# Performance work log

Hardware: AMD Instinct MI355X
Metric: run time of the kernel (lower is better)

## Reference

```python
import jax, jax.numpy as jnp
import numpy as np

N = 100000      # nodes
E = 1600000     # edges (avg degree 16)
K = 3           # num_stacks
T = 4           # num_layers
H = 16          # hidden channels (conv1 out)
C = 1           # num_classes
BN_EPS = 1e-5


def setup_inputs() -> dict:
    key = jax.random.key(0)
    ks = jax.random.split(key, 14)
    s = 0.1
    return {
        "x": jax.random.normal(ks[0], (N, 1), jnp.float32),
        "edge_index": jax.random.randint(ks[1], (2, E), 0, N, dtype=jnp.int64),
        "edge_weight": jax.random.uniform(ks[2], (E,), jnp.float32),
        # conv1 (ARMAConv 1->16, K stacks, shared weights)
        "w1_init": jax.random.normal(ks[3], (K, 1, H), jnp.float32) * s,
        "w1_w":    jax.random.normal(ks[4], (K, H, H), jnp.float32) * s,
        "w1_root": jax.random.normal(ks[5], (K, 1, H), jnp.float32) * s,
        "w1_b":    jax.random.normal(ks[6], (K, H), jnp.float32) * s,
        "bn1_g": jnp.ones((H,), jnp.float32),
        "bn1_b": jnp.zeros((H,), jnp.float32),
        # conv2 (ARMAConv 16->1, act=None)
        "w2_init": jax.random.normal(ks[7], (K, H, C), jnp.float32) * s,
        "w2_w":    jax.random.normal(ks[8], (K, C, C), jnp.float32) * s,
        "w2_root": jax.random.normal(ks[9], (K, H, C), jnp.float32) * s,
        "w2_b":    jax.random.normal(ks[10], (K, C), jnp.float32) * s,
        # end linear 1->1
        "lin_w": jax.random.normal(ks[11], (C, C), jnp.float32) * s,
        "lin_b": jnp.zeros((C,), jnp.float32),
    }


def _arma_conv(x, src, dst, norm, init_w, w, root_w, bias, act):
    """PyG ARMAConv with shared weights. x: [N,Fin] -> [N,Fout]."""
    n = x.shape[0]
    # root/skip term (dropout is identity in eval); bias broadcast per stack
    root = jnp.einsum('ni,kio->nko', x, root_w) + bias[None, :, :]  # [N,K,Fout]
    out = jnp.einsum('ni,kio->nko', x, init_w)                      # t=0 transform
    for t in range(T):
        if t > 0:
            out = jnp.einsum('nki,kio->nko', out, w)                # shared weight
        msg = out[src] * norm[:, None, None]                        # [E,K,Fout]
        out = jax.ops.segment_sum(msg, dst, num_segments=n)         # A_hat @ out
        out = out + root
        if act:
            out = jax.nn.relu(out)
    return out.mean(axis=1)  # average over stacks


def reference(x, edge_index, edge_weight, w1_init, w1_w, w1_root, w1_b,
              bn1_g, bn1_b, w2_init, w2_w, w2_root, w2_b, lin_w, lin_b):
    src, dst = edge_index[0], edge_index[1]
    n = x.shape[0]
    # gcn_norm without self loops
    deg = jax.ops.segment_sum(edge_weight, dst, num_segments=n)
    dis = jnp.where(deg > 0, 1.0 / jnp.sqrt(deg), 0.0)
    norm = dis[src] * edge_weight * dis[dst]

    h = _arma_conv(x, src, dst, norm, w1_init, w1_w, w1_root, w1_b, act=True)
    # BatchNorm1d over node dim (batch statistics, deterministic)
    mu = h.mean(axis=0)
    var = h.var(axis=0)
    h = (h - mu) / jnp.sqrt(var + BN_EPS) * bn1_g + bn1_b
    h = jax.nn.relu(h)
    # dropout is identity in eval
    h = _arma_conv(h, src, dst, norm, w2_init, w2_w, w2_root, w2_b, act=False)
    h = h @ lin_w.T + lin_b
    return jax.nn.sigmoid(h)
```

## Files before the change

kernel.cpp:

```cpp
#include <hip/hip_runtime.h>
#include <hip/hip_bf16.h>
#include <hip/hip_fp16.h>
#include <math.h>

#define CAP 44

__device__ __forceinline__ float pk_w(unsigned pk) {
    return __half2float(__ushort_as_half((unsigned short)(pk >> 17)));
}
__device__ __forceinline__ unsigned pk_make(int s, float w) {
    unsigned hb = (unsigned)__half_as_ushort(__float2half_rn(w));
    return (unsigned)s | (hb << 17);
}


__global__ void zero_kernel(float* p, int n) {
    int i = blockIdx.x * blockDim.x + threadIdx.x;
    if (i < n) p[i] = 0.f;
}

__global__ void bucket_insert_part(const int* __restrict__ ei, const float* __restrict__ ew,
                                   int* __restrict__ len, unsigned* __restrict__ pcsr,
                                   int E, int n) {
    int part = blockIdx.x & 7;
    int chunk = blockIdx.x >> 3;
    int base = chunk * 2048;
    int pw = (n + 7) >> 3;
    int lo = part * pw;
    int hi = lo + pw; hi = hi < n ? hi : n;
    int end = base + 2048; end = end < E ? end : E;
    for (int i = base + threadIdx.x; i < end; i += 256) {
        int d = __builtin_nontemporal_load(ei + E + i);
        if (d >= lo && d < hi) {
            int s = __builtin_nontemporal_load(ei + i);
            float w = __builtin_nontemporal_load(ew + i);
            int pos = atomicAdd(&len[d], 1);
            if (pos < CAP) pcsr[d * CAP + pos] = pk_make(s, w);
        }
    }
}

__global__ void wdeg_dis_w(const unsigned* __restrict__ pcsr, const int* __restrict__ len,
                           const float* __restrict__ x, float2* __restrict__ dx, int n) {
    int wid = (int)((blockIdx.x * blockDim.x + threadIdx.x) >> 6);
    int lane = threadIdx.x & 63;
    if (wid >= n) return;
    int L = len[wid]; L = L < CAP ? L : CAP;
    float w = (lane < L) ? pk_w(pcsr[wid * CAP + lane]) : 0.f;
#pragma unroll
    for (int off = 32; off >= 1; off >>= 1) w += __shfl_xor(w, off, 64);
    if (lane == 0) {
        float d = (w > 0.f) ? (1.0f / sqrtf(w)) : 0.f;
        dx[wid] = make_float2(d, x[wid]);
    }
}

__global__ void normagg_init(unsigned* __restrict__ pcsr, const int* __restrict__ len,
                             const float2* __restrict__ dx,
                             const float* __restrict__ w_init, const float* __restrict__ w_root,
                             const float* __restrict__ w_b,
                             __hip_bfloat16* __restrict__ P, int n) {
    int wid = (int)((blockIdx.x * blockDim.x + threadIdx.x) >> 6);
    int lane = threadIdx.x & 63;
    if (wid >= n) return;
    int L = len[wid]; L = L < CAP ? L : CAP;
    float2 d0 = dx[wid];
    float dn = d0.x, xv = d0.y;
    float part = 0.f;
    if (lane < L) {
        int idx = wid * CAP + lane;
        unsigned pk = pcsr[idx];
        int s = (int)(pk & 0x1FFFFu);
        float w = pk_w(pk);
        float2 sdx = dx[s];
        float wn = w * dn * sdx.x;
        pcsr[idx] = pk_make(s, wn);
        part = wn * sdx.y;
    }
#pragma unroll
    for (int off = 32; off >= 1; off >>= 1) part += __shfl_xor(part, off, 64);
    if (lane < 48) {
        float v = fmaxf(part * w_init[lane] + xv * w_root[lane] + w_b[lane], 0.f);
        P[(unsigned)wid * 64u + lane] = __float2bfloat16(v);
    }
}


template<int LAST>
__global__ void __launch_bounds__(256) agg48p(
    const __hip_bfloat16* __restrict__ P, const float* __restrict__ W,
    const float2* __restrict__ dx, const float* __restrict__ w_root,
    const float* __restrict__ w_b, const int* __restrict__ len,
    const unsigned* __restrict__ pcsr, __hip_bfloat16* __restrict__ Pout, int n) {
    int wid = (int)((blockIdx.x * blockDim.x + threadIdx.x) >> 6);
    int lane = threadIdx.x & 63;
    if (wid >= n || lane >= 48) return;
    int k = lane >> 4, o = lane & 15;
    float wv[16];
#pragma unroll
    for (int i = 0; i < 16; i++) wv[i] = W[k * 256 + i * 16 + o];

    int p = wid * CAP;
    int L = len[wid]; L = L < CAP ? L : CAP;
    int end = p + L;
    float a0 = 0.f, a1 = 0.f, a2 = 0.f, a3 = 0.f;
    for (; p + 15 < end; p += 16) {
        unsigned e[16];
#pragma unroll
        for (int j = 0; j < 16; j++) e[j] = pcsr[p + j];
        float q[16];
#pragma unroll
        for (int j = 0; j < 16; j++)
            q[j] = __bfloat162float(P[(e[j] & 0x1FFFFu) * 64u + lane]);
#pragma unroll
        for (int j = 0; j < 4; j++) {
            a0 += q[4 * j]     * pk_w(e[4 * j]);
            a1 += q[4 * j + 1] * pk_w(e[4 * j + 1]);
            a2 += q[4 * j + 2] * pk_w(e[4 * j + 2]);
            a3 += q[4 * j + 3] * pk_w(e[4 * j + 3]);
        }
    }
    for (; p + 7 < end; p += 8) {
        unsigned e[8];
#pragma unroll
        for (int j = 0; j < 8; j++) e[j] = pcsr[p + j];
        float q[8];
#pragma unroll
        for (int j = 0; j < 8; j++)
            q[j] = __bfloat162float(P[(e[j] & 0x1FFFFu) * 64u + lane]);
#pragma unroll
        for (int j = 0; j < 2; j++) {
            a0 += q[4 * j]     * pk_w(e[4 * j]);
            a1 += q[4 * j + 1] * pk_w(e[4 * j + 1]);
            a2 += q[4 * j + 2] * pk_w(e[4 * j + 2]);
            a3 += q[4 * j + 3] * pk_w(e[4 * j + 3]);
        }
    }
    for (; p + 3 < end; p += 4) {
        unsigned e[4];
#pragma unroll
        for (int j = 0; j < 4; j++) e[j] = pcsr[p + j];
#pragma unroll
        for (int j = 0; j < 4; j++) {
            float q = __bfloat162float(P[(e[j] & 0x1FFFFu) * 64u + lane]);
            (j == 0 ? a0 : j == 1 ? a1 : j == 2 ? a2 : a3) += q * pk_w(e[j]);
        }
    }
    for (; p < end; p++) {
        unsigned e = pcsr[p];
        a0 += __bfloat162float(P[(e & 0x1FFFFu) * 64u + lane]) * pk_w(e);
    }
    float S = (a0 + a1) + (a2 + a3);

    float acc = 0.f;
    int bl = lane & 48;
#pragma unroll
    for (int i = 0; i < 16; i++) {
        float sv = __shfl(S, bl + i, 64);
        acc += sv * wv[i];
    }
    float v = fmaxf(acc + dx[wid].y * w_root[lane] + w_b[lane], 0.f);
    if (LAST) {
        float h = v + __shfl(v, lane + 16, 64) + __shfl(v, lane + 32, 64);
        if (lane < 16)
            Pout[(unsigned)wid * 16u + lane] = __float2bfloat16(h * (1.f / 3.f));
    } else {
        Pout[(unsigned)wid * 64u + lane] = __float2bfloat16(v);
    }
}


__global__ void bn_stats16(const __hip_bfloat16* __restrict__ H, float* __restrict__ acc, int n) {
    int tid = threadIdx.x;
    int c = tid & 15;
    int rowSlot = (int)((blockIdx.x * blockDim.x + tid) >> 4);
    int rowStride = (int)((gridDim.x * blockDim.x) >> 4);
    float s1 = 0.f, s2 = 0.f;
    for (int r = rowSlot; r < n; r += rowStride) {
        float h = __bfloat162float(H[(unsigned)r * 16u + c]);
        s1 += h;
        s2 += h * h;
    }
    __shared__ float sh[256];
    sh[tid] = s1; __syncthreads();
    for (int off = 128; off >= 16; off >>= 1) { if (tid < off) sh[tid] += sh[tid + off]; __syncthreads(); }
    if (tid < 16) atomicAdd(&acc[tid], sh[tid]);
    __syncthreads();
    sh[tid] = s2; __syncthreads();
    for (int off = 128; off >= 16; off >>= 1) { if (tid < off) sh[tid] += sh[tid + off]; __syncthreads(); }
    if (tid < 16) atomicAdd(&acc[16 + tid], sh[tid]);
}

__global__ void bn_cvec(const float* __restrict__ acc, const float* __restrict__ g,
                        const float* __restrict__ b, int n,
                        const float* __restrict__ w2w, const float* __restrict__ w2i,
                        const float* __restrict__ w2r, const float* __restrict__ w2b,
                        float* __restrict__ coef, float* __restrict__ cvec) {
    int c = threadIdx.x;
    const float inv3 = 1.f / 3.f;
    if (c < 16) {
        float mu = acc[c] / (float)n;
        float var = acc[16 + c] / (float)n - mu * mu;
        float sc = g[c] / sqrtf(var + 1e-5f);
        coef[c] = sc;
        coef[16 + c] = b[c] - mu * sc;
        float wk0 = w2w[0], wk1 = w2w[1], wk2 = w2w[2];
        float wks[3] = {wk0, wk1, wk2};
        float psi = 0.f, r3 = 0.f, r2 = 0.f, r1 = 0.f, r0 = 0.f;
#pragma unroll
        for (int k = 0; k < 3; k++) {
            float w = wks[k], w2_ = w * w, w3 = w2_ * w;
            psi += w3 * w2i[k * 16 + c];
            float rr = w2r[k * 16 + c];
            r3 += w3 * rr; r2 += w2_ * rr; r1 += w * rr; r0 += rr;
        }
        cvec[c] = psi * inv3;
        cvec[16 + c] = r3 * inv3;
        cvec[32 + c] = r2 * inv3;
        cvec[48 + c] = r1 * inv3;
        cvec[64 + c] = r0 * inv3;
    } else if (c == 16) {
        float wk0 = w2w[0], wk1 = w2w[1], wk2 = w2w[2];
        float wks[3] = {wk0, wk1, wk2};
        float b3 = 0.f, b2 = 0.f, b1 = 0.f, b0 = 0.f;
#pragma unroll
        for (int k = 0; k < 3; k++) {
            float w = wks[k], w2_ = w * w, w3 = w2_ * w;
            float bb = w2b[k];
            b3 += w3 * bb; b2 += w2_ * bb; b1 += w * bb; b0 += bb;
        }
        cvec[80] = b3 * inv3; cvec[81] = b2 * inv3; cvec[82] = b1 * inv3; cvec[83] = b0 * inv3;
    }
}


__global__ void conv2_init16(const __hip_bfloat16* __restrict__ H, const float* __restrict__ coef,
                             const float* __restrict__ cvec,
                             float* __restrict__ z, float4* __restrict__ R, int n) {
    unsigned node = blockIdx.x * blockDim.x + threadIdx.x;
    if (node >= (unsigned)n) return;
    const __hip_bfloat16* row = &H[node * 16u];
    float zz = 0.f, r3 = cvec[80], r2 = cvec[81], r1 = cvec[82], r0 = cvec[83];
#pragma unroll
    for (int c = 0; c < 16; c++) {
        float h = __bfloat162float(row[c]);
        float hb = fmaxf(h * coef[c] + coef[16 + c], 0.f);
        zz += hb * cvec[c];
        r3 += hb * cvec[16 + c];
        r2 += hb * cvec[32 + c];
        r1 += hb * cvec[48 + c];
        r0 += hb * cvec[64 + c];
    }
    z[node] = zz;
    R[node] = make_float4(r3, r2, r1, r0);
}

template<int FINAL>
__global__ void horner(const float* __restrict__ zin, const float* __restrict__ R, int comp,
                       const int* __restrict__ len, const unsigned* __restrict__ pcsr,
                       float* __restrict__ zout, const float* __restrict__ lw,
                       const float* __restrict__ lb, int n) {
    int node = blockIdx.x * blockDim.x + threadIdx.x;
    if (node >= n) return;
    int p = node * CAP;
    int L = len[node]; L = L < CAP ? L : CAP;
    int end = p + L;
    float a0 = 0.f, a1 = 0.f;
    for (; p + 15 < end; p += 16) {
        unsigned e[16];
#pragma unroll
        for (int j = 0; j < 16; j++) e[j] = pcsr[p + j];
        float q[16];
#pragma unroll
        for (int j = 0; j < 16; j++) q[j] = zin[e[j] & 0x1FFFFu];
#pragma unroll
        for (int j = 0; j < 8; j++) {
            a0 += q[2 * j] * pk_w(e[2 * j]);
            a1 += q[2 * j + 1] * pk_w(e[2 * j + 1]);
        }
    }
    for (; p + 7 < end; p += 8) {
        unsigned e[8];
#pragma unroll
        for (int j = 0; j < 8; j++) e[j] = pcsr[p + j];
#pragma unroll
        for (int j = 0; j < 8; j++) {
            float q = zin[e[j] & 0x1FFFFu];
            (j & 1 ? a1 : a0) += q * pk_w(e[j]);
        }
    }
    for (; p < end; p++) {
        unsigned e = pcsr[p];
        a0 += zin[e & 0x1FFFFu] * pk_w(e);
    }
    float v = (a0 + a1) + R[(unsigned)node * 4u + comp];
    if (FINAL) {
        float t = v * lw[0] + lb[0];
        zout[node] = 1.f / (1.f + expf(-t));
    } else {
        zout[node] = v;
    }
}


extern "C" void kernel_launch(void* const* d_in, const int* in_sizes, int n_in,
                              void* d_out, int out_size, void* d_ws, size_t ws_size,
                              hipStream_t stream) {
    const float* x = (const float*)d_in[0];
    const int* ei = (const int*)d_in[1];
    const float* ew = (const float*)d_in[2];
    const float* w1_init = (const float*)d_in[3];
    const float* w1_w = (const float*)d_in[4];
    const float* w1_root = (const float*)d_in[5];
    const float* w1_b = (const float*)d_in[6];
    const float* bn1_g = (const float*)d_in[7];
    const float* bn1_b = (const float*)d_in[8];
    const float* w2_init = (const float*)d_in[9];
    const float* w2_w = (const float*)d_in[10];
    const float* w2_root = (const float*)d_in[11];
    const float* w2_b = (const float*)d_in[12];
    const float* lin_w = (const float*)d_in[13];
    const float* lin_b = (const float*)d_in[14];

    const int N = in_sizes[0];
    const int E = in_sizes[2];
    float* out = (float*)d_out;

    char* ws = (char*)d_ws;
    size_t off = 0;
    auto alloc = [&](size_t bytes) {
        void* p = ws + off;
        off += (bytes + 15) & ~(size_t)15;
        return p;
    };
    int*   len     = (int*)  alloc((size_t)N * 4);
    float* bn_acc  = (float*)alloc(32 * 4);
    float* bn_coef = (float*)alloc(32 * 4);
    float* cvec    = (float*)alloc(96 * 4);
    float2* dx     = (float2*)alloc((size_t)N * 8);
    float* zA      = (float*)alloc((size_t)N * 4);
    float* zB      = (float*)alloc((size_t)N * 4);
    float4* Rbuf   = (float4*)alloc((size_t)N * 16);
    unsigned* pcsr = (unsigned*)alloc((size_t)N * CAP * 4);
    __hip_bfloat16* bufP = (__hip_bfloat16*)alloc((size_t)N * 64 * 2);
    __hip_bfloat16* bufQ = (__hip_bfloat16*)alloc((size_t)N * 64 * 2);
    __hip_bfloat16* hbuf = bufQ;
    (void)ws_size;

    const int BS = 256;
    int gN = (N + BS - 1) / BS;
    int gW = (N + 3) / 4;

    zero_kernel<<<(N + 32 + BS - 1) / BS, BS, 0, stream>>>((float*)len, N + 32);

    int nChunks = (E + 2047) / 2048;
    bucket_insert_part<<<8 * nChunks, BS, 0, stream>>>(ei, ew, len, pcsr, E, N);
    wdeg_dis_w<<<gW, BS, 0, stream>>>(pcsr, len, x, dx, N);
    normagg_init<<<gW, BS, 0, stream>>>(pcsr, len, dx, w1_init, w1_root, w1_b, bufP, N);

    agg48p<0><<<gW, BS, 0, stream>>>(bufP, w1_w, dx, w1_root, w1_b, len, pcsr, bufQ, N);
    agg48p<0><<<gW, BS, 0, stream>>>(bufQ, w1_w, dx, w1_root, w1_b, len, pcsr, bufP, N);
    agg48p<1><<<gW, BS, 0, stream>>>(bufP, w1_w, dx, w1_root, w1_b, len, pcsr, hbuf, N);

    bn_stats16<<<512, 256, 0, stream>>>(hbuf, bn_acc, N);
    bn_cvec<<<1, 64, 0, stream>>>(bn_acc, bn1_g, bn1_b, N, w2_w, w2_init, w2_root, w2_b,
                                  bn_coef, cvec);

    conv2_init16<<<gN, BS, 0, stream>>>(hbuf, bn_coef, cvec, zA, Rbuf, N);
    horner<0><<<gN, BS, 0, stream>>>(zA, (const float*)Rbuf, 0, len, pcsr, zB, lin_w, lin_b, N);
    horner<0><<<gN, BS, 0, stream>>>(zB, (const float*)Rbuf, 1, len, pcsr, zA, lin_w, lin_b, N);
    horner<0><<<gN, BS, 0, stream>>>(zA, (const float*)Rbuf, 2, len, pcsr, zB, lin_w, lin_b, N);
    horner<1><<<gN, BS, 0, stream>>>(zB, (const float*)Rbuf, 3, len, pcsr, out, lin_w, lin_b, N);
}
```

Baseline: 393.7 us.

## Fuse first conv layer into gather from scalar node features, persistent bucket insert

The t=0 layer no longer writes a 48-wide bf16 feature buffer. normagg_y stores only the per-node aggregated scalar plus x, and a new agg_t1 kernel rebuilds the relu'd layer-0 features on the fly from each neighbour's float2, then does the t=1 aggregation and transform. This cuts one full 48-channel gather pass and its bf16 write and read, at the cost of extra FMAs per edge. The bucket insert becomes a persistent grid of 256 blocks over 32 edge slices, agg48p gets a launch-bounds occupancy hint, and its 4-wide remainder loop is dropped.

```diff
diff --git a/kernel.cpp b/kernel.cpp
--- a/kernel.cpp
+++ b/kernel.cpp
@@ -19,16 +19,17 @@
     if (i < n) p[i] = 0.f;
 }
 
-__global__ void bucket_insert_part(const int* __restrict__ ei, const float* __restrict__ ew,
-                                   int* __restrict__ len, unsigned* __restrict__ pcsr,
-                                   int E, int n) {
+__global__ void __launch_bounds__(256, 1) bucket_insert_pers(
+        const int* __restrict__ ei, const float* __restrict__ ew,
+        int* __restrict__ len, unsigned* __restrict__ pcsr, int E, int n) {
     int part = blockIdx.x & 7;
-    int chunk = blockIdx.x >> 3;
-    int base = chunk * 2048;
+    int slot = blockIdx.x >> 3;
     int pw = (n + 7) >> 3;
     int lo = part * pw;
     int hi = lo + pw; hi = hi < n ? hi : n;
-    int end = base + 2048; end = end < E ? end : E;
+    int epb = (E + 31) >> 5;
+    int base = slot * epb;
+    int end = base + epb; end = end < E ? end : E;
     for (int i = base + threadIdx.x; i < end; i += 256) {
         int d = __builtin_nontemporal_load(ei + E + i);
         if (d >= lo && d < hi) {
@@ -55,17 +56,14 @@
     }
 }
 
-__global__ void normagg_init(unsigned* __restrict__ pcsr, const int* __restrict__ len,
-                             const float2* __restrict__ dx,
-                             const float* __restrict__ w_init, const float* __restrict__ w_root,
-                             const float* __restrict__ w_b,
-                             __hip_bfloat16* __restrict__ P, int n) {
+__global__ void normagg_y(unsigned* __restrict__ pcsr, const int* __restrict__ len,
+                          const float2* __restrict__ dx, float2* __restrict__ yx, int n) {
     int wid = (int)((blockIdx.x * blockDim.x + threadIdx.x) >> 6);
     int lane = threadIdx.x & 63;
     if (wid >= n) return;
     int L = len[wid]; L = L < CAP ? L : CAP;
     float2 d0 = dx[wid];
-    float dn = d0.x, xv = d0.y;
+    float dn = d0.x;
     float part = 0.f;
     if (lane < L) {
         int idx = wid * CAP + lane;
@@ -79,15 +77,67 @@
     }
 #pragma unroll
     for (int off = 32; off >= 1; off >>= 1) part += __shfl_xor(part, off, 64);
-    if (lane < 48) {
-        float v = fmaxf(part * w_init[lane] + xv * w_root[lane] + w_b[lane], 0.f);
-        P[(unsigned)wid * 64u + lane] = __float2bfloat16(v);
-    }
-}
-
+    if (lane == 0) yx[wid] = make_float2(part, d0.y);
+}
+
+
+__global__ void __launch_bounds__(256) agg_t1(
+    const float2* __restrict__ yx, const float* __restrict__ W,
+    const float* __restrict__ w_init, const float* __restrict__ w_root,
+    const float* __restrict__ w_b, const int* __restrict__ len,
+    const unsigned* __restrict__ pcsr, __hip_bfloat16* __restrict__ Pout, int n) {
+    int wid = (int)((blockIdx.x * blockDim.x + threadIdx.x) >> 6);
+    int lane = threadIdx.x & 63;
+    if (wid >= n || lane >= 48) return;
+    int k = lane >> 4, o = lane & 15;
+    float wv[16];
+#pragma unroll
+    for (int i = 0; i < 16; i++) wv[i] = W[k * 256 + i * 16 + o];
+    float wi_c = w_init[lane], wr_c = w_root[lane], b_c = w_b[lane];
+
+    int p = wid * CAP;
+    int L = len[wid]; L = L < CAP ? L : CAP;
+    int end = p + L;
+    float a0 = 0.f, a1 = 0.f, a2 = 0.f, a3 = 0.f;
+    for (; p + 15 < end; p += 16) {
+        unsigned e[16];
+#pragma unroll
+        for (int j = 0; j < 16; j++) e[j] = pcsr[p + j];
+        float2 g[16];
+#pragma unroll
+        for (int j = 0; j < 16; j++) g[j] = yx[e[j] & 0x1FFFFu];
+#pragma unroll
+        for (int j = 0; j < 4; j++) {
+#pragma unroll
+            for (int m = 0; m < 4; m++) {
+                int jj = 4 * j + m;
+                float q = fmaxf(g[jj].x * wi_c + g[jj].y * wr_c + b_c, 0.f);
+                (m == 0 ? a0 : m == 1 ? a1 : m == 2 ? a2 : a3) += q * pk_w(e[jj]);
+            }
+        }
+    }
+    for (; p < end; p++) {
+        unsigned e = pcsr[p];
+        float2 g = yx[e & 0x1FFFFu];
+        float q = fmaxf(g.x * wi_c + g.y * wr_c + b_c, 0.f);
+        a0 += q * pk_w(e);
+    }
+    float S = (a0 + a1) + (a2 + a3);
+
+    float acc = 0.f;
+    int bl = lane & 48;
+#pragma unroll
+    for (int i = 0; i < 16; i++) {
+        float sv = __shfl(S, bl + i, 64);
+        acc += sv * wv[i];
+    }
+    float xv = yx[wid].y;
+    float v = fmaxf(acc + xv * wr_c + b_c, 0.f);
+    Pout[(unsigned)wid * 64u + lane] = __float2bfloat16(v);
+}
 
 template<int LAST>
-__global__ void __launch_bounds__(256) agg48p(
+__global__ void __launch_bounds__(256, 3) agg48p(
     const __hip_bfloat16* __restrict__ P, const float* __restrict__ W,
     const float2* __restrict__ dx, const float* __restrict__ w_root,
     const float* __restrict__ w_b, const int* __restrict__ len,
@@ -134,16 +184,6 @@
             a1 += q[4 * j + 1] * pk_w(e[4 * j + 1]);
             a2 += q[4 * j + 2] * pk_w(e[4 * j + 2]);
             a3 += q[4 * j + 3] * pk_w(e[4 * j + 3]);
-        }
-    }
-    for (; p + 3 < end; p += 4) {
-        unsigned e[4];
-#pragma unroll
-        for (int j = 0; j < 4; j++) e[j] = pcsr[p + j];
-#pragma unroll
-        for (int j = 0; j < 4; j++) {
-            float q = __bfloat162float(P[(e[j] & 0x1FFFFu) * 64u + lane]);
-            (j == 0 ? a0 : j == 1 ? a1 : j == 2 ? a2 : a3) += q * pk_w(e[j]);
         }
     }
     for (; p < end; p++) {
@@ -338,6 +378,7 @@
     float* bn_coef = (float*)alloc(32 * 4);
     float* cvec    = (float*)alloc(96 * 4);
     float2* dx     = (float2*)alloc((size_t)N * 8);
+    float2* yx     = (float2*)alloc((size_t)N * 8);
     float* zA      = (float*)alloc((size_t)N * 4);
     float* zB      = (float*)alloc((size_t)N * 4);
     float4* Rbuf   = (float4*)alloc((size_t)N * 16);
@@ -353,14 +394,13 @@
 
     zero_kernel<<<(N + 32 + BS - 1) / BS, BS, 0, stream>>>((float*)len, N + 32);
 
-    int nChunks = (E + 2047) / 2048;
-    bucket_insert_part<<<8 * nChunks, BS, 0, stream>>>(ei, ew, len, pcsr, E, N);
+    bucket_insert_pers<<<256, BS, 0, stream>>>(ei, ew, len, pcsr, E, N);
     wdeg_dis_w<<<gW, BS, 0, stream>>>(pcsr, len, x, dx, N);
-    normagg_init<<<gW, BS, 0, stream>>>(pcsr, len, dx, w1_init, w1_root, w1_b, bufP, N);
-
+    normagg_y<<<gW, BS, 0, stream>>>(pcsr, len, dx, yx, N);
+
+    agg_t1<<<gW, BS, 0, stream>>>(yx, w1_w, w1_init, w1_root, w1_b, len, pcsr, bufP, N);
     agg48p<0><<<gW, BS, 0, stream>>>(bufP, w1_w, dx, w1_root, w1_b, len, pcsr, bufQ, N);
-    agg48p<0><<<gW, BS, 0, stream>>>(bufQ, w1_w, dx, w1_root, w1_b, len, pcsr, bufP, N);
-    agg48p<1><<<gW, BS, 0, stream>>>(bufP, w1_w, dx, w1_root, w1_b, len, pcsr, hbuf, N);
+    agg48p<1><<<gW, BS, 0, stream>>>(bufQ, w1_w, dx, w1_root, w1_b, len, pcsr, hbuf, N);
 
     bn_stats16<<<512, 256, 0, stream>>>(hbuf, bn_acc, N);
     bn_cvec<<<1, 64, 0, stream>>>(bn_acc, bn1_g, bn1_b, N, w2_w, w2_init, w2_root, w2_b,
```

Result: slower. 667.2 us (+69.4%).
